# Kernel tuning notes

Measured on AMD Instinct MI355X. Metric: run time of the kernel, lower is better.

Reference implementation:

```python
import jax, jax.numpy as jnp
import numpy as np

N_NODES = 50000
N_EDGES = 400000
HEADS = 3
CH = 128
NEG_SLOPE = 0.2
EPS = 1e-16


def setup_inputs() -> dict:
    key = jax.random.key(0)
    ks = jax.random.split(key, 10)
    return {
        "x": jax.random.normal(ks[0], (N_NODES, 9), jnp.float32),
        "emb_w": jax.random.normal(ks[1], (9, 128), jnp.float32) * 0.1,
        "emb_b": jax.random.normal(ks[2], (128,), jnp.float32) * 0.1,
        "gat_w": jax.random.normal(ks[3], (128, HEADS * CH), jnp.float32) * 0.05,
        "att_src": jax.random.normal(ks[4], (HEADS, CH), jnp.float32) * 0.1,
        "att_dst": jax.random.normal(ks[5], (HEADS, CH), jnp.float32) * 0.1,
        "gat_bias": jax.random.normal(ks[6], (CH,), jnp.float32) * 0.1,
        "out_w": jax.random.normal(ks[7], (128, 4), jnp.float32) * 0.1,
        "out_b": jax.random.normal(ks[8], (4,), jnp.float32) * 0.1,
        "edge_index": jax.random.randint(ks[9], (2, N_EDGES), 0, N_NODES, jnp.int64 if jax.config.jax_enable_x64 else jnp.int32),
    }


def reference(x, emb_w, emb_b, gat_w, att_src, att_dst, gat_bias, out_w, out_b, edge_index):
    n = x.shape[0]
    h = x @ emb_w + emb_b                                   # [N,128]
    # add self loops (PyG GATConv default)
    loops = jnp.arange(n, dtype=edge_index.dtype)
    src = jnp.concatenate([edge_index[0], loops])
    dst = jnp.concatenate([edge_index[1], loops])
    xh = (h @ gat_w).reshape(n, HEADS, CH)                  # [N,H,C]
    a_src = jnp.einsum('nhc,hc->nh', xh, att_src)           # [N,H]
    a_dst = jnp.einsum('nhc,hc->nh', xh, att_dst)           # [N,H]
    e = a_src[src] + a_dst[dst]                             # [E,H]
    e = jax.nn.leaky_relu(e, NEG_SLOPE)
    # segment softmax over destination node
    e_max = jax.ops.segment_max(e, dst, num_segments=n)
    e = jnp.exp(e - e_max[dst])
    denom = jax.ops.segment_sum(e, dst, num_segments=n)
    alpha = e / (denom[dst] + EPS)                          # [E,H]
    msg = xh[src] * alpha[:, :, None]                       # [E,H,C]
    agg = jax.ops.segment_sum(msg, dst, num_segments=n)     # [N,H,C]
    out = agg.mean(axis=1) + gat_bias                       # concat=False -> head mean
    x_new = out + h                                         # residual
    return x_new @ out_w + out_b                            # [N,4]
```

## Files before the change

### kernel.cpp

```cpp
#include <hip/hip_runtime.h>
#include <hip/hip_bf16.h>
#include <cstdint>

#define NEG 0.2f
#define SBS 256
#define SCAN2_T 1024
#define PADK 56

typedef __attribute__((ext_vector_type(8))) short bf16x8;
typedef __attribute__((ext_vector_type(8))) unsigned short ushort8;
typedef __attribute__((ext_vector_type(4))) float f32x4;

__device__ __forceinline__ float bf2f(unsigned short u){
  return __uint_as_float(((unsigned)u)<<16);
}
__device__ __forceinline__ unsigned short f2bf(float f){
  __hip_bfloat16 b = __float2bfloat16(f);
  return *reinterpret_cast<unsigned short*>(&b);
}

__global__ __launch_bounds__(256)
void prep_kernel(const float* __restrict__ gat_w, const float* __restrict__ att_src,
                 const float* __restrict__ att_dst, float* __restrict__ w_att_s,
                 float* __restrict__ w_att_d, unsigned short* __restrict__ Bt2)
{
  if (blockIdx.x < 192){
    int wave = threadIdx.x >> 6, lane = threadIdx.x & 63;
    int o = blockIdx.x*4 + wave;
    if (o >= 768) return;
    int isD = (o >= 384);
    int t = isD ? (o - 384) : o;
    int h = t >> 7, k = t & 127;
    const float* att = isD ? att_dst : att_src;
    int c = 2*lane;
    float g0 = gat_w[(size_t)k*384 + h*128 + c];
    float g1 = gat_w[(size_t)k*384 + h*128 + c + 1];
    float dot = g0*att[h*128+c] + g1*att[h*128+c+1];
    #pragma unroll
    for (int off=32; off; off>>=1) dot += __shfl_down(dot, off);
    if (lane==0){
      if (isD) w_att_d[t] = dot; else w_att_s[t] = dot;
    }
  } else {
    int i = (blockIdx.x-192)*256 + threadIdx.x;
    if (i >= 12*128*32) return;
    int ks  = i >> 12;
    int rem = i & 4095;
    int col = rem >> 5;
    int kk  = rem & 31;
    int t = ks*32 + kk;
    int h = t >> 7, k = t & 127;
    Bt2[i] = f2bf(gat_w[(size_t)k*384 + h*128 + col] * (1.f/3.f));
  }
}

__global__ __launch_bounds__(256)
void embed_kernel(const float* __restrict__ x, const float* __restrict__ emb_w,
                  const float* __restrict__ emb_b, const float* __restrict__ w_att_s,
                  const float* __restrict__ w_att_d,
                  unsigned short* __restrict__ h_bf, float* __restrict__ a_s,
                  float* __restrict__ a_d, int nN)
{
  int n = blockIdx.x*256 + threadIdx.x;
  if (n >= nN) return;

  float xv[9];
  #pragma unroll
  for (int k=0;k<9;k++) xv[k] = x[(size_t)n*9 + k];

  float s0=0.f,s1=0.f,s2=0.f, d0=0.f,d1=0.f,d2=0.f;
  unsigned short* hrow = h_bf + (size_t)n*128;

  #pragma unroll 4
  for (int c0=0; c0<128; c0+=8){
    unsigned short pk[8];
    #pragma unroll
    for (int j=0;j<8;j++){
      int c = c0 + j;
      float acc = emb_b[c];
      #pragma unroll
      for (int k=0;k<9;k++) acc += xv[k]*emb_w[k*128+c];
      pk[j] = f2bf(acc);
      s0 += acc*w_att_s[c]; s1 += acc*w_att_s[128+c]; s2 += acc*w_att_s[256+c];
      d0 += acc*w_att_d[c]; d1 += acc*w_att_d[128+c]; d2 += acc*w_att_d[256+c];
    }
    *(int4*)(hrow + c0) = *(int4*)pk;
  }
  a_s[(size_t)n*3+0]=s0; a_s[(size_t)n*3+1]=s1; a_s[(size_t)n*3+2]=s2;
  a_d[(size_t)n*3+0]=d0; a_d[(size_t)n*3+1]=d1; a_d[(size_t)n*3+2]=d2;
}

__global__ __launch_bounds__(256)
void deg_kernel(const int* __restrict__ ei, int* __restrict__ deg, int nE)
{
  int e = blockIdx.x*256 + threadIdx.x;
  if (e < nE) atomicAdd(&deg[ei[nE + e]], 1);
}

__global__ __launch_bounds__(SBS)
void blocksum_kernel(const int* __restrict__ deg, int* __restrict__ bsum, int nN)
{
  int i = blockIdx.x*SBS + threadIdx.x;
  int v = (i < nN) ? deg[i] : 0;
  #pragma unroll
  for (int off=32; off; off>>=1) v += __shfl_down(v, off);
  __shared__ int ws[SBS/64];
  if ((threadIdx.x&63)==0) ws[threadIdx.x>>6] = v;
  __syncthreads();
  if (threadIdx.x==0){
    int s=0;
    #pragma unroll
    for (int i2=0;i2<SBS/64;i2++) s += ws[i2];
    bsum[blockIdx.x]=s;
  }
}

__global__ __launch_bounds__(SCAN2_T)
void scansum_kernel(const int* __restrict__ bsum, int* __restrict__ boff, int nB)
{
  __shared__ int s[SCAN2_T];
  int t = threadIdx.x;
  int v = (t < nB) ? bsum[t] : 0;
  s[t] = v;
  __syncthreads();
  for (int off=1; off<SCAN2_T; off<<=1){
    int add = (t >= off) ? s[t-off] : 0;
    __syncthreads();
    s[t] += add;
    __syncthreads();
  }
  if (t < nB) boff[t] = (t==0) ? 0 : s[t-1];
}

__global__ __launch_bounds__(SBS)
void blockscan_kernel(const int* __restrict__ deg, const int* __restrict__ boff,
                      int* __restrict__ rowptr, int* __restrict__ cursor, int nN)
{
  __shared__ int s[SBS];
  int t = threadIdx.x;
  int i = blockIdx.x*SBS + t;
  int v = (i < nN) ? deg[i] : 0;
  s[t] = v;
  __syncthreads();
  for (int off=1; off<SBS; off<<=1){
    int add = (t >= off) ? s[t-off] : 0;
    __syncthreads();
    s[t] += add;
    __syncthreads();
  }
  int excl = boff[blockIdx.x] + ((t==0) ? 0 : s[t-1]);
  if (i < nN){ rowptr[i] = excl; cursor[i] = excl; }
  if (i == nN-1) rowptr[nN] = excl + v;
}

__global__ __launch_bounds__(256)
void scatter_kernel(const int* __restrict__ ei, int* __restrict__ cursor,
                    int* __restrict__ csr, int nE)
{
  int e = blockIdx.x*256 + threadIdx.x;
  if (e < nE){
    int s = ei[e], d = ei[nE + e];
    int pos = atomicAdd(&cursor[d], 1);
    csr[pos] = s;
  }
}

__global__ __launch_bounds__(256)
void gather_kernel(const int* __restrict__ rowptr, const int* __restrict__ csr,
                   const float* __restrict__ a_s, const float* __restrict__ a_d,
                   const unsigned short* __restrict__ h_bf,
                   unsigned short* __restrict__ hagg, int nN)
{
  int wave = threadIdx.x >> 6, lane = threadIdx.x & 63;
  int g   = lane >> 4;
  int lin = lane & 15;
  int gb  = lane & 48;
  int n = blockIdx.x*16 + wave*4 + g;
  int valid = (n < nN);
  int nc = valid ? n : (nN-1);

  int ro  = rowptr[nc];
  int deg = rowptr[nc+1] - ro;
  int degT = valid ? (deg + 1) : 0;

  float ad0 = a_d[(size_t)nc*3+0], ad1 = a_d[(size_t)nc*3+1], ad2 = a_d[(size_t)nc*3+2];

  float acc0[8], acc1[8], acc2[8];
  #pragma unroll
  for (int c=0;c<8;c++){ acc0[c]=0.f; acc1[c]=0.f; acc2[c]=0.f; }
  float d0=0.f, d1=0.f, d2=0.f;

  const unsigned short* hb8 = h_bf + 8*lin;

  for (int base=0; base<degT; base+=16){
    int i = base + lin;
    int sReg = nc; float p0=0.f, p1=0.f, p2=0.f;
    if (i < degT){
      int s = (i < deg) ? csr[ro+i] : nc;
      sReg = s;
      float e0 = a_s[(size_t)s*3+0] + ad0; e0 = e0>0.f ? e0 : NEG*e0;
      float e1 = a_s[(size_t)s*3+1] + ad1; e1 = e1>0.f ? e1 : NEG*e1;
      float e2 = a_s[(size_t)s*3+2] + ad2; e2 = e2>0.f ? e2 : NEG*e2;
      p0 = __expf(e0); p1 = __expf(e1); p2 = __expf(e2);
      d0 += p0; d1 += p1; d2 += p2;
    }
    int cnt = min(16, degT - base);
    int j = 0;
    for (; j+1 < cnt; j += 2){
      int   sA = __shfl(sReg, gb+j);
      int   sB = __shfl(sReg, gb+j+1);
      float A0 = __shfl(p0, gb+j),   A1 = __shfl(p1, gb+j),   A2 = __shfl(p2, gb+j);
      float B0 = __shfl(p0, gb+j+1), B1 = __shfl(p1, gb+j+1), B2 = __shfl(p2, gb+j+1);
      ushort8 ha = *(const ushort8*)(hb8 + (size_t)sA*128);
      ushort8 hb = *(const ushort8*)(hb8 + (size_t)sB*128);
      #pragma unroll
      for (int c=0;c<8;c++){
        float fa = bf2f(ha[c]);
        float fb = bf2f(hb[c]);
        acc0[c] += A0*fa + B0*fb;
        acc1[c] += A1*fa + B1*fb;
        acc2[c] += A2*fa + B2*fb;
      }
    }
    if (j < cnt){
      int   sA = __shfl(sReg, gb+j);
      float A0 = __shfl(p0, gb+j), A1 = __shfl(p1, gb+j), A2 = __shfl(p2, gb+j);
      ushort8 ha = *(const ushort8*)(hb8 + (size_t)sA*128);
      #pragma unroll
      for (int c=0;c<8;c++){
        float fa = bf2f(ha[c]);
        acc0[c] += A0*fa; acc1[c] += A1*fa; acc2[c] += A2*fa;
      }
    }
  }

  #pragma unroll
  for (int off=1; off<16; off<<=1){
    d0 += __shfl_xor(d0, off);
    d1 += __shfl_xor(d1, off);
    d2 += __shfl_xor(d2, off);
  }

  if (valid){
    float w0 = 1.f/(d0+1e-16f);
    float w1 = 1.f/(d1+1e-16f);
    float w2 = 1.f/(d2+1e-16f);
    unsigned short o0[8], o1[8], o2[8];
    #pragma unroll
    for (int c=0;c<8;c++){
      o0[c] = f2bf(acc0[c]*w0);
      o1[c] = f2bf(acc1[c]*w1);
      o2[c] = f2bf(acc2[c]*w2);
    }
    size_t bidx = (size_t)n*384 + 8*lin;
    *(int4*)(hagg + bidx      ) = *(int4*)o0;
    *(int4*)(hagg + bidx + 128) = *(int4*)o1;
    *(int4*)(hagg + bidx + 256) = *(int4*)o2;
  }
}

__global__ __launch_bounds__(256)
void gemm2_kernel(const unsigned short* __restrict__ hagg,
                  const unsigned short* __restrict__ Bt2,
                  const unsigned short* __restrict__ h_bf,
                  const float* __restrict__ gat_bias,
                  const float* __restrict__ out_w, const float* __restrict__ out_b,
                  float* __restrict__ out, int nN)
{
  __shared__ __align__(16) unsigned short Bs[2][128*PADK];
  int tid  = threadIdx.x;
  int wave = tid >> 6, lane = tid & 63;
  int cl = lane & 15, kg = lane >> 4;
  int r0 = blockIdx.x*64 + wave*16;
  int rowA = min(r0 + cl, nN-1);
  const unsigned short* aBase = hagg + (size_t)rowA*384 + kg*8;

  int scol = tid >> 1, shalf = tid & 1;
  int dstI = scol*(PADK/8) + shalf*2;

  {
    const int4* src = (const int4*)Bt2;
    int4 t0 = src[2*tid], t1 = src[2*tid+1];
    ((int4*)Bs[0])[dstI]   = t0;
    ((int4*)Bs[0])[dstI+1] = t1;
  }
  f32x4 acc[8];
  #pragma unroll
  for (int f=0;f<8;f++) acc[f] = (f32x4){0.f,0.f,0.f,0.f};
  bf16x8 aCur = *(const bf16x8*)(aBase);
  __syncthreads();

  #pragma unroll
  for (int ks=0; ks<12; ks++){
    int4 t0, t1; bf16x8 aNext;
    if (ks < 11){
      const int4* src = (const int4*)(Bt2 + (size_t)(ks+1)*4096);
      t0 = src[2*tid]; t1 = src[2*tid+1];
      aNext = *(const bf16x8*)(aBase + (ks+1)*32);
    }
    const unsigned short* bs = Bs[ks & 1];
    #pragma unroll
    for (int f=0;f<8;f++){
      bf16x8 b = *(const bf16x8*)(bs + (f*16 + cl)*PADK + kg*8);
      acc[f] = __builtin_amdgcn_mfma_f32_16x16x32_bf16(aCur, b, acc[f], 0, 0, 0);
    }
    if (ks < 11){
      int4* dst = (int4*)Bs[(ks+1) & 1];
      dst[dstI]   = t0;
      dst[dstI+1] = t1;
      aCur = aNext;
    }
    __syncthreads();
  }

  float p[4][4];
  #pragma unroll
  for (int r=0;r<4;r++)
    #pragma unroll
    for (int j=0;j<4;j++) p[r][j]=0.f;

  #pragma unroll
  for (int f=0;f<8;f++){
    int col = f*16 + cl;
    float bias = gat_bias[col];
    float w0=out_w[col*4+0], w1=out_w[col*4+1], w2=out_w[col*4+2], w3=out_w[col*4+3];
    #pragma unroll
    for (int r=0;r<4;r++){
      int row = r0 + kg*4 + r;
      float hres = (row < nN) ? bf2f(h_bf[(size_t)row*128 + col]) : 0.f;
      float xn = acc[f][r] + bias + hres;
      p[r][0] += xn*w0; p[r][1] += xn*w1; p[r][2] += xn*w2; p[r][3] += xn*w3;
    }
  }
  #pragma unroll
  for (int off=1; off<16; off<<=1){
    #pragma unroll
    for (int r=0;r<4;r++)
      #pragma unroll
      for (int j=0;j<4;j++) p[r][j] += __shfl_xor(p[r][j], off);
  }
  if (cl == 0){
    #pragma unroll
    for (int r=0;r<4;r++){
      int row = r0 + kg*4 + r;
      if (row < nN){
        float4 o = {p[r][0]+out_b[0], p[r][1]+out_b[1], p[r][2]+out_b[2], p[r][3]+out_b[3]};
        *(float4*)(out + (size_t)row*4) = o;
      }
    }
  }
}

extern "C" void kernel_launch(void* const* d_in, const int* in_sizes, int n_in,
                              void* d_out, int out_size, void* d_ws, size_t ws_size,
                              hipStream_t stream) {
  const float* x       = (const float*)d_in[0];
  const float* emb_w   = (const float*)d_in[1];
  const float* emb_b   = (const float*)d_in[2];
  const float* gat_w   = (const float*)d_in[3];
  const float* att_src = (const float*)d_in[4];
  const float* att_dst = (const float*)d_in[5];
  const float* gat_bias= (const float*)d_in[6];
  const float* out_w   = (const float*)d_in[7];
  const float* out_b   = (const float*)d_in[8];
  const int*   ei      = (const int*)d_in[9];
  float* out = (float*)d_out;

  int nN = in_sizes[0]/9;
  int nE = in_sizes[9]/2;
  int nB = (nN + SBS - 1) / SBS;

  char* p = (char*)d_ws;
  auto alloc = [&](size_t bytes)->char*{
    char* r = p; p += (bytes + 255) & ~(size_t)255; return r;
  };
  unsigned short* h_bf   = (unsigned short*)alloc((size_t)nN*128*2);
  float*          a_s    = (float*)         alloc((size_t)nN*3*4);
  float*          a_d    = (float*)         alloc((size_t)nN*3*4);
  float*          w_att_s= (float*)         alloc(384*4);
  float*          w_att_d= (float*)         alloc(384*4);
  unsigned short* Bt2    = (unsigned short*)alloc((size_t)12*128*32*2);
  int*            deg    = (int*)           alloc((size_t)nN*4);
  int*            rowptr = (int*)           alloc(((size_t)nN+1)*4);
  int*            cursor = (int*)           alloc((size_t)nN*4);
  int*            csr    = (int*)           alloc((size_t)nE*4);
  int*            bsum   = (int*)           alloc((size_t)nB*4);
  int*            boff   = (int*)           alloc((size_t)nB*4);
  unsigned short* hagg   = (unsigned short*)alloc((size_t)nN*384*2);

  hipMemsetAsync(deg, 0, (size_t)nN*4, stream);

  prep_kernel<<<384, 256, 0, stream>>>(gat_w, att_src, att_dst, w_att_s, w_att_d, Bt2);

  embed_kernel<<<(nN+255)/256, 256, 0, stream>>>(
      x, emb_w, emb_b, w_att_s, w_att_d, h_bf, a_s, a_d, nN);

  deg_kernel<<<(nE+255)/256, 256, 0, stream>>>(ei, deg, nE);
  blocksum_kernel<<<nB, SBS, 0, stream>>>(deg, bsum, nN);
  scansum_kernel<<<1, SCAN2_T, 0, stream>>>(bsum, boff, nB);
  blockscan_kernel<<<nB, SBS, 0, stream>>>(deg, boff, rowptr, cursor, nN);
  scatter_kernel<<<(nE+255)/256, 256, 0, stream>>>(ei, cursor, csr, nE);

  gather_kernel<<<(nN+15)/16, 256, 0, stream>>>(
      rowptr, csr, a_s, a_d, h_bf, hagg, nN);

  gemm2_kernel<<<(nN+63)/64, 256, 0, stream>>>(
      hagg, Bt2, h_bf, gat_bias, out_w, out_b, out, nN);
}
```

Baseline: 210.5 us.

## Fuse prep into embed/deg kernels, drop memset and blocksum, widen gather lanes

The attention-weight projection now runs inside every embed block, which stores it in shared memory and also zeroes deg and bsum, so the memset and prep kernel go away. The Bt2 transposed-weight build moves into extra blocks of the degree kernel. That kernel also atomically accumulates per-block sums, which removes the blocksum kernel, and the scan shrinks to 256 threads. The gather kernel now uses 8 lanes per node with 16 channels each instead of 16 lanes with 8, doubling nodes per block. In exchange, each embed block redundantly computes 768 dot products of length 128, bsum takes contended atomics, and the scan assumes at most 256 blocks.

```diff
diff --git a/kernel.cpp b/kernel.cpp
--- a/kernel.cpp
+++ b/kernel.cpp
@@ -4,7 +4,6 @@
 
 #define NEG 0.2f
 #define SBS 256
-#define SCAN2_T 1024
 #define PADK 56
 
 typedef __attribute__((ext_vector_type(8))) short bf16x8;
@@ -20,48 +19,34 @@
 }
 
 __global__ __launch_bounds__(256)
-void prep_kernel(const float* __restrict__ gat_w, const float* __restrict__ att_src,
-                 const float* __restrict__ att_dst, float* __restrict__ w_att_s,
-                 float* __restrict__ w_att_d, unsigned short* __restrict__ Bt2)
-{
-  if (blockIdx.x < 192){
-    int wave = threadIdx.x >> 6, lane = threadIdx.x & 63;
-    int o = blockIdx.x*4 + wave;
-    if (o >= 768) return;
+void embed_kernel(const float* __restrict__ x, const float* __restrict__ emb_w,
+                  const float* __restrict__ emb_b, const float* __restrict__ gat_w,
+                  const float* __restrict__ att_src, const float* __restrict__ att_dst,
+                  unsigned short* __restrict__ h_bf, float* __restrict__ a_s,
+                  float* __restrict__ a_d, int* __restrict__ deg,
+                  int* __restrict__ bsum, int nN)
+{
+  __shared__ float watt[768];
+  int tid = threadIdx.x;
+
+  #pragma unroll
+  for (int r=0;r<3;r++){
+    int o = tid + r*256;
     int isD = (o >= 384);
-    int t = isD ? (o - 384) : o;
-    int h = t >> 7, k = t & 127;
-    const float* att = isD ? att_dst : att_src;
-    int c = 2*lane;
-    float g0 = gat_w[(size_t)k*384 + h*128 + c];
-    float g1 = gat_w[(size_t)k*384 + h*128 + c + 1];
-    float dot = g0*att[h*128+c] + g1*att[h*128+c+1];
-    #pragma unroll
-    for (int off=32; off; off>>=1) dot += __shfl_down(dot, off);
-    if (lane==0){
-      if (isD) w_att_d[t] = dot; else w_att_s[t] = dot;
-    }
-  } else {
-    int i = (blockIdx.x-192)*256 + threadIdx.x;
-    if (i >= 12*128*32) return;
-    int ks  = i >> 12;
-    int rem = i & 4095;
-    int col = rem >> 5;
-    int kk  = rem & 31;
-    int t = ks*32 + kk;
-    int h = t >> 7, k = t & 127;
-    Bt2[i] = f2bf(gat_w[(size_t)k*384 + h*128 + col] * (1.f/3.f));
-  }
-}
-
-__global__ __launch_bounds__(256)
-void embed_kernel(const float* __restrict__ x, const float* __restrict__ emb_w,
-                  const float* __restrict__ emb_b, const float* __restrict__ w_att_s,
-                  const float* __restrict__ w_att_d,
-                  unsigned short* __restrict__ h_bf, float* __restrict__ a_s,
-                  float* __restrict__ a_d, int nN)
-{
-  int n = blockIdx.x*256 + threadIdx.x;
+    int t2 = isD ? (o-384) : o;
+    int h = t2 >> 7, k = t2 & 127;
+    const float* att = isD ? (att_dst + h*128) : (att_src + h*128);
+    const float* gw  = gat_w + (size_t)k*384 + h*128;
+    float dot = 0.f;
+    #pragma unroll 8
+    for (int c=0;c<128;c++) dot += gw[c]*att[c];
+    watt[o] = dot;
+  }
+  __syncthreads();
+
+  int n = blockIdx.x*256 + tid;
+  if (n < nN) deg[n] = 0;
+  if (tid == 0) bsum[blockIdx.x] = 0;
   if (n >= nN) return;
 
   float xv[9];
@@ -81,8 +66,8 @@
       #pragma unroll
       for (int k=0;k<9;k++) acc += xv[k]*emb_w[k*128+c];
       pk[j] = f2bf(acc);
-      s0 += acc*w_att_s[c]; s1 += acc*w_att_s[128+c]; s2 += acc*w_att_s[256+c];
-      d0 += acc*w_att_d[c]; d1 += acc*w_att_d[128+c]; d2 += acc*w_att_d[256+c];
+      s0 += acc*watt[c]; s1 += acc*watt[128+c]; s2 += acc*watt[256+c];
+      d0 += acc*watt[384+c]; d1 += acc*watt[512+c]; d2 += acc*watt[640+c];
     }
     *(int4*)(hrow + c0) = *(int4*)pk;
   }
@@ -91,39 +76,40 @@
 }
 
 __global__ __launch_bounds__(256)
-void deg_kernel(const int* __restrict__ ei, int* __restrict__ deg, int nE)
-{
-  int e = blockIdx.x*256 + threadIdx.x;
-  if (e < nE) atomicAdd(&deg[ei[nE + e]], 1);
-}
-
-__global__ __launch_bounds__(SBS)
-void blocksum_kernel(const int* __restrict__ deg, int* __restrict__ bsum, int nN)
-{
-  int i = blockIdx.x*SBS + threadIdx.x;
-  int v = (i < nN) ? deg[i] : 0;
-  #pragma unroll
-  for (int off=32; off; off>>=1) v += __shfl_down(v, off);
-  __shared__ int ws[SBS/64];
-  if ((threadIdx.x&63)==0) ws[threadIdx.x>>6] = v;
-  __syncthreads();
-  if (threadIdx.x==0){
-    int s=0;
-    #pragma unroll
-    for (int i2=0;i2<SBS/64;i2++) s += ws[i2];
-    bsum[blockIdx.x]=s;
-  }
-}
-
-__global__ __launch_bounds__(SCAN2_T)
+void deg_kernel(const int* __restrict__ ei, int* __restrict__ deg,
+                int* __restrict__ bsum, const float* __restrict__ gat_w,
+                unsigned short* __restrict__ Bt2, int nE, int ebN)
+{
+  if (blockIdx.x < (unsigned)ebN){
+    int e = blockIdx.x*256 + threadIdx.x;
+    if (e < nE){
+      int d = ei[nE + e];
+      atomicAdd(&deg[d], 1);
+      atomicAdd(&bsum[d>>8], 1);
+    }
+  } else {
+    int i = (blockIdx.x - ebN)*256 + threadIdx.x;
+    if (i < 12*128*32){
+      int ks  = i >> 12;
+      int rem = i & 4095;
+      int col = rem >> 5;
+      int kk  = rem & 31;
+      int t = ks*32 + kk;
+      int h = t >> 7, k = t & 127;
+      Bt2[i] = f2bf(gat_w[(size_t)k*384 + h*128 + col] * (1.f/3.f));
+    }
+  }
+}
+
+__global__ __launch_bounds__(256)
 void scansum_kernel(const int* __restrict__ bsum, int* __restrict__ boff, int nB)
 {
-  __shared__ int s[SCAN2_T];
+  __shared__ int s[256];
   int t = threadIdx.x;
   int v = (t < nB) ? bsum[t] : 0;
   s[t] = v;
   __syncthreads();
-  for (int off=1; off<SCAN2_T; off<<=1){
+  for (int off=1; off<256; off<<=1){
     int add = (t >= off) ? s[t-off] : 0;
     __syncthreads();
     s[t] += add;
@@ -172,10 +158,10 @@
                    unsigned short* __restrict__ hagg, int nN)
 {
   int wave = threadIdx.x >> 6, lane = threadIdx.x & 63;
-  int g   = lane >> 4;
-  int lin = lane & 15;
-  int gb  = lane & 48;
-  int n = blockIdx.x*16 + wave*4 + g;
+  int g   = lane >> 3;
+  int lin = lane & 7;
+  int gb  = lane & 56;
+  int n = blockIdx.x*32 + wave*8 + g;
   int valid = (n < nN);
   int nc = valid ? n : (nN-1);
 
@@ -185,14 +171,14 @@
 
   float ad0 = a_d[(size_t)nc*3+0], ad1 = a_d[(size_t)nc*3+1], ad2 = a_d[(size_t)nc*3+2];
 
-  float acc0[8], acc1[8], acc2[8];
-  #pragma unroll
-  for (int c=0;c<8;c++){ acc0[c]=0.f; acc1[c]=0.f; acc2[c]=0.f; }
+  float a0[16], a1[16], a2[16];
+  #pragma unroll
+  for (int c=0;c<16;c++){ a0[c]=0.f; a1[c]=0.f; a2[c]=0.f; }
   float d0=0.f, d1=0.f, d2=0.f;
 
-  const unsigned short* hb8 = h_bf + 8*lin;
-
-  for (int base=0; base<degT; base+=16){
+  const unsigned short* hb = h_bf + 16*lin;
+
+  for (int base=0; base<degT; base+=8){
     int i = base + lin;
     int sReg = nc; float p0=0.f, p1=0.f, p2=0.f;
     if (i < degT){
@@ -204,38 +190,52 @@
       p0 = __expf(e0); p1 = __expf(e1); p2 = __expf(e2);
       d0 += p0; d1 += p1; d2 += p2;
     }
-    int cnt = min(16, degT - base);
+    int cnt = min(8, degT - base);
     int j = 0;
     for (; j+1 < cnt; j += 2){
       int   sA = __shfl(sReg, gb+j);
       int   sB = __shfl(sReg, gb+j+1);
       float A0 = __shfl(p0, gb+j),   A1 = __shfl(p1, gb+j),   A2 = __shfl(p2, gb+j);
       float B0 = __shfl(p0, gb+j+1), B1 = __shfl(p1, gb+j+1), B2 = __shfl(p2, gb+j+1);
-      ushort8 ha = *(const ushort8*)(hb8 + (size_t)sA*128);
-      ushort8 hb = *(const ushort8*)(hb8 + (size_t)sB*128);
+      const unsigned short* ra = hb + (size_t)sA*128;
+      const unsigned short* rb = hb + (size_t)sB*128;
+      ushort8 ha0 = *(const ushort8*)(ra), ha1 = *(const ushort8*)(ra+8);
+      ushort8 hb0 = *(const ushort8*)(rb), hb1 = *(const ushort8*)(rb+8);
       #pragma unroll
       for (int c=0;c<8;c++){
-        float fa = bf2f(ha[c]);
-        float fb = bf2f(hb[c]);
-        acc0[c] += A0*fa + B0*fb;
-        acc1[c] += A1*fa + B1*fb;
-        acc2[c] += A2*fa + B2*fb;
+        float fa = bf2f(ha0[c]), fb = bf2f(hb0[c]);
+        a0[c] += A0*fa + B0*fb;
+        a1[c] += A1*fa + B1*fb;
+        a2[c] += A2*fa + B2*fb;
+      }
+      #pragma unroll
+      for (int c=0;c<8;c++){
+        float fa = bf2f(ha1[c]), fb = bf2f(hb1[c]);
+        a0[8+c] += A0*fa + B0*fb;
+        a1[8+c] += A1*fa + B1*fb;
+        a2[8+c] += A2*fa + B2*fb;
       }
     }
     if (j < cnt){
       int   sA = __shfl(sReg, gb+j);
       float A0 = __shfl(p0, gb+j), A1 = __shfl(p1, gb+j), A2 = __shfl(p2, gb+j);
-      ushort8 ha = *(const ushort8*)(hb8 + (size_t)sA*128);
+      const unsigned short* ra = hb + (size_t)sA*128;
+      ushort8 ha0 = *(const ushort8*)(ra), ha1 = *(const ushort8*)(ra+8);
       #pragma unroll
       for (int c=0;c<8;c++){
-        float fa = bf2f(ha[c]);
-        acc0[c] += A0*fa; acc1[c] += A1*fa; acc2[c] += A2*fa;
+        float fa = bf2f(ha0[c]);
+        a0[c] += A0*fa; a1[c] += A1*fa; a2[c] += A2*fa;
       }
-    }
-  }
-
-  #pragma unroll
-  for (int off=1; off<16; off<<=1){
+      #pragma unroll
+      for (int c=0;c<8;c++){
+        float fa = bf2f(ha1[c]);
+        a0[8+c] += A0*fa; a1[8+c] += A1*fa; a2[8+c] += A2*fa;
+      }
+    }
+  }
+
+  #pragma unroll
+  for (int off=1; off<8; off<<=1){
     d0 += __shfl_xor(d0, off);
     d1 += __shfl_xor(d1, off);
     d2 += __shfl_xor(d2, off);
@@ -245,17 +245,20 @@
     float w0 = 1.f/(d0+1e-16f);
     float w1 = 1.f/(d1+1e-16f);
     float w2 = 1.f/(d2+1e-16f);
-    unsigned short o0[8], o1[8], o2[8];
-    #pragma unroll
-    for (int c=0;c<8;c++){
-      o0[c] = f2bf(acc0[c]*w0);
-      o1[c] = f2bf(acc1[c]*w1);
-      o2[c] = f2bf(acc2[c]*w2);
-    }
-    size_t bidx = (size_t)n*384 + 8*lin;
-    *(int4*)(hagg + bidx      ) = *(int4*)o0;
-    *(int4*)(hagg + bidx + 128) = *(int4*)o1;
-    *(int4*)(hagg + bidx + 256) = *(int4*)o2;
+    unsigned short o0[16], o1[16], o2[16];
+    #pragma unroll
+    for (int c=0;c<16;c++){
+      o0[c] = f2bf(a0[c]*w0);
+      o1[c] = f2bf(a1[c]*w1);
+      o2[c] = f2bf(a2[c]*w2);
+    }
+    size_t bi = (size_t)n*384 + 16*lin;
+    *(int4*)(hagg + bi      ) = *(int4*)(o0);
+    *(int4*)(hagg + bi +   8) = *(int4*)(o0+8);
+    *(int4*)(hagg + bi + 128) = *(int4*)(o1);
+    *(int4*)(hagg + bi + 136) = *(int4*)(o1+8);
+    *(int4*)(hagg + bi + 256) = *(int4*)(o2);
+    *(int4*)(hagg + bi + 264) = *(int4*)(o2+8);
   }
 }
 
@@ -369,6 +372,7 @@
   int nN = in_sizes[0]/9;
   int nE = in_sizes[9]/2;
   int nB = (nN + SBS - 1) / SBS;
+  int ebN = (nE + 255)/256;
 
   char* p = (char*)d_ws;
   auto alloc = [&](size_t bytes)->char*{
@@ -377,8 +381,6 @@
   unsigned short* h_bf   = (unsigned short*)alloc((size_t)nN*128*2);
   float*          a_s    = (float*)         alloc((size_t)nN*3*4);
   float*          a_d    = (float*)         alloc((size_t)nN*3*4);
-  float*          w_att_s= (float*)         alloc(384*4);
-  float*          w_att_d= (float*)         alloc(384*4);
   unsigned short* Bt2    = (unsigned short*)alloc((size_t)12*128*32*2);
   int*            deg    = (int*)           alloc((size_t)nN*4);
   int*            rowptr = (int*)           alloc(((size_t)nN+1)*4);
@@ -388,20 +390,16 @@
   int*            boff   = (int*)           alloc((size_t)nB*4);
   unsigned short* hagg   = (unsigned short*)alloc((size_t)nN*384*2);
 
-  hipMemsetAsync(deg, 0, (size_t)nN*4, stream);
-
-  prep_kernel<<<384, 256, 0, stream>>>(gat_w, att_src, att_dst, w_att_s, w_att_d, Bt2);
-
-  embed_kernel<<<(nN+255)/256, 256, 0, stream>>>(
-      x, emb_w, emb_b, w_att_s, w_att_d, h_bf, a_s, a_d, nN);
-
-  deg_kernel<<<(nE+255)/256, 256, 0, stream>>>(ei, deg, nE);
-  blocksum_kernel<<<nB, SBS, 0, stream>>>(deg, bsum, nN);
-  scansum_kernel<<<1, SCAN2_T, 0, stream>>>(bsum, boff, nB);
+  embed_kernel<<<nB, 256, 0, stream>>>(
+      x, emb_w, emb_b, gat_w, att_src, att_dst, h_bf, a_s, a_d, deg, bsum, nN);
+
+  deg_kernel<<<ebN + 192, 256, 0, stream>>>(ei, deg, bsum, gat_w, Bt2, nE, ebN);
+
+  scansum_kernel<<<1, 256, 0, stream>>>(bsum, boff, nB);
   blockscan_kernel<<<nB, SBS, 0, stream>>>(deg, boff, rowptr, cursor, nN);
-  scatter_kernel<<<(nE+255)/256, 256, 0, stream>>>(ei, cursor, csr, nE);
-
-  gather_kernel<<<(nN+15)/16, 256, 0, stream>>>(
+  scatter_kernel<<<ebN, 256, 0, stream>>>(ei, cursor, csr, nE);
+
+  gather_kernel<<<(nN+31)/32, 256, 0, stream>>>(
       rowptr, csr, a_s, a_d, h_bf, hagg, nN);
 
   gemm2_kernel<<<(nN+63)/64, 256, 0, stream>>>(
```

Result: slower. 431.4 us (+105.0%).
